# Optimization experiments

Measured on AMD Instinct MI355X. Metric: run time of the kernel, lower is better.

Reference implementation:

```python
import jax, jax.numpy as jnp
import numpy as np

FS, R, ULAW = 160, 2, 256  # frame_size, n_samples_per_step, 2**ulaw


def _conv1d(x, w, b):
    # x: [B,C,L], w: [O,I,3], VALID conv (PyTorch Conv1d, no padding)
    y = jax.lax.conv_general_dilated(x, w, (1,), 'VALID',
                                     dimension_numbers=('NCH', 'OIH', 'NCH'))
    return y + b[None, :, None]


def _gru(x, Wih, Whh, bih, bhh):
    # PyTorch GRU (batch_first), gate order r,z,n. x: [B,T,In] -> [B,T,H]
    B = x.shape[0]
    H = Whh.shape[1]
    xW = jnp.einsum('bti,gi->btg', x, Wih) + bih  # precompute input gates [B,T,3H]
    def step(h, xw):
        gh = h @ Whh.T + bhh
        r = jax.nn.sigmoid(xw[:, :H] + gh[:, :H])
        z = jax.nn.sigmoid(xw[:, H:2 * H] + gh[:, H:2 * H])
        n = jnp.tanh(xw[:, 2 * H:] + r * gh[:, 2 * H:])
        h = (1.0 - z) * n + z * h
        return h, h
    h0 = jnp.zeros((B, H), x.dtype)
    _, ys = jax.lax.scan(step, h0, jnp.swapaxes(xW, 0, 1))
    return jnp.swapaxes(ys, 0, 1)


def _mdense(x, w1, w2, b1, b2, f1, f2):
    return jnp.tanh(x @ w1.T + b1) * f1 + jnp.tanh(x @ w2.T + b2) * f2


def setup_inputs() -> dict:
    key = jax.random.key(0)
    ks = jax.random.split(key, 40)
    B, NF, NBF = 64, 15, 20
    T = (NF - 4) * FS  # 1760: two VALID k=3 convs -> 11 frames
    EP, ES, DF, H1, H2 = 64, 128, 128, 384, 16
    IN_A = 3 * ES * R + DF   # 896
    IN_B = H1 + DF           # 512
    p = lambda k, shape, s=0.1: (s * jax.random.normal(k, shape)).astype(jnp.float32)
    d = {
        'in_data': jax.random.randint(ks[0], (B, T, 3), 0, ULAW),
        'features': jax.random.normal(ks[1], (B, NF, NBF), jnp.float32),
        'periods': jax.random.randint(ks[2], (B, NF, 1), 0, 256),
        'targets': jax.random.randint(ks[3], (B, T), 0, ULAW),
        'embed_pitch': p(ks[4], (256, EP)),
        'embed_sig': p(ks[5], (ULAW, ES)),
        'conv1_w': p(ks[6], (DF, EP + NBF, 3)), 'conv1_b': p(ks[7], (DF,)),
        'conv2_w': p(ks[8], (DF, DF, 3)), 'conv2_b': p(ks[9], (DF,)),
        'fd1_w': p(ks[10], (DF, DF)), 'fd1_b': p(ks[11], (DF,)),
        'fd2_w': p(ks[12], (DF, DF)), 'fd2_b': p(ks[13], (DF,)),
        'ga_wih': p(ks[14], (3 * H1, IN_A)), 'ga_whh': p(ks[15], (3 * H1, H1)),
        'ga_bih': p(ks[16], (3 * H1,)), 'ga_bhh': p(ks[17], (3 * H1,)),
        'gb_wih': p(ks[18], (3 * H2, IN_B)), 'gb_whh': p(ks[19], (3 * H2, H2)),
        'gb_bih': p(ks[20], (3 * H2,)), 'gb_bhh': p(ks[21], (3 * H2,)),
        'md1_w1': p(ks[22], (ULAW, H2)), 'md1_w2': p(ks[23], (ULAW, H2)),
        'md1_b1': p(ks[24], (ULAW,)), 'md1_b2': p(ks[25], (ULAW,)),
        'md1_f1': jnp.ones((ULAW,), jnp.float32), 'md1_f2': jnp.ones((ULAW,), jnp.float32),
        'md2_w1': p(ks[26], (ULAW, H2 + ES)), 'md2_w2': p(ks[27], (ULAW, H2 + ES)),
        'md2_b1': p(ks[28], (ULAW,)), 'md2_b2': p(ks[29], (ULAW,)),
        'md2_f1': jnp.ones((ULAW,), jnp.float32), 'md2_f2': jnp.ones((ULAW,), jnp.float32),
    }
    return d


def reference(in_data, features, periods, targets, embed_pitch, embed_sig,
              conv1_w, conv1_b, conv2_w, conv2_b, fd1_w, fd1_b, fd2_w, fd2_b,
              ga_wih, ga_whh, ga_bih, ga_bhh, gb_wih, gb_whh, gb_bih, gb_bhh,
              md1_w1, md1_w2, md1_b1, md1_b2, md1_f1, md1_f2,
              md2_w1, md2_w2, md2_b1, md2_b2, md2_f1, md2_f2):
    B, T = targets.shape
    # frame-rate feature network
    pitch = embed_pitch[periods[..., 0]]                  # [B,15,EP]
    cat = jnp.concatenate([features, pitch], axis=-1)      # [B,15,NBF+EP]
    x = jnp.swapaxes(cat, 1, 2)                            # [B,C,15]
    x = jnp.tanh(_conv1d(x, conv1_w, conv1_b))
    x = jnp.tanh(_conv1d(x, conv2_w, conv2_b))             # [B,DF,11]
    f = jnp.swapaxes(x, 1, 2)
    f = jnp.tanh(f @ fd1_w.T + fd1_b)
    f = jnp.tanh(f @ fd2_w.T + fd2_b)                      # [B,11,DF]
    rep = jnp.repeat(f, FS // R, axis=1)                   # [B,880,DF]
    # sample-rate network (bunched: R samples per step)
    emb = embed_sig[in_data].reshape(B, T, -1).reshape(B, T // R, -1)  # [B,880,3*ES*R]
    rnn_in = jnp.concatenate([emb, rep], axis=-1)
    g1 = _gru(rnn_in, ga_wih, ga_whh, ga_bih, ga_bhh)      # [B,880,H1]
    g2 = _gru(jnp.concatenate([g1, rep], axis=-1), gb_wih, gb_whh, gb_bih, gb_bhh)  # [B,880,H2]
    o1 = _mdense(g2, md1_w1, md1_w2, md1_b1, md1_b2, md1_f1, md1_f2)  # [B,880,ULAW]
    # teacher forcing (p_teacher_forcing = 1.0): even-index targets feed branch 2
    pred_exc = targets[:, 0::R]                            # [B,880]
    ctx = jnp.concatenate([g2, embed_sig[pred_exc]], axis=-1)
    o2 = _mdense(ctx, md2_w1, md2_w2, md2_b1, md2_b2, md2_f1, md2_f2)
    # strided scatter: out[:, ::2]=o1, out[:, 1::2]=o2 == interleave
    out = jnp.stack([o1, o2], axis=2).reshape(B, T, ULAW)
    return out
```

## Files before the change

### kernel.cpp

```cpp
#include <hip/hip_runtime.h>
#include <hip/hip_bf16.h>
#include <hip/hip_fp16.h>

#define NF    15
#define NBF   20
#define TT    1760
#define TS    880
#define EP    64
#define ES    128
#define DF    128
#define H1    384
#define G3    1152
#define INA   896
#define JREP  11

typedef _Float16 h2v __attribute__((ext_vector_type(2)));

__device__ __forceinline__ float sigmf_(float x){ return 1.0f/(1.0f + __expf(-x)); }
__device__ __forceinline__ float tanhf_(float x){ return 2.0f/(1.0f + __expf(-2.0f*x)) - 1.0f; }
__device__ __forceinline__ h2v bc_h2(unsigned u){ return __builtin_bit_cast(h2v, u); }
__device__ __forceinline__ float fdot2_(h2v a, h2v b, float c){
#if __has_builtin(__builtin_amdgcn_fdot2)
  return __builtin_amdgcn_fdot2(a, b, c, false);
#else
  return c + (float)a[0]*(float)b[0] + (float)a[1]*(float)b[1];
#endif
}
__device__ __forceinline__ unsigned pk2_(float a, float b){
#if __has_builtin(__builtin_amdgcn_cvt_pkrtz)
  return __builtin_bit_cast(unsigned, __builtin_amdgcn_cvt_pkrtz(a, b));
#else
  unsigned lo = (unsigned)__builtin_bit_cast(unsigned short, (_Float16)a);
  unsigned hi = (unsigned)__builtin_bit_cast(unsigned short, (_Float16)b);
  return lo | (hi << 16);
#endif
}
__device__ __forceinline__ void bar_lgkm(){
  asm volatile("s_waitcnt lgkmcnt(0)" ::: "memory");
  __builtin_amdgcn_s_barrier();
  __builtin_amdgcn_sched_barrier(0);
}

__global__ __launch_bounds__(128) void k_frame(const float* feat, const int* periods, const float* embp,
   const float* c1w, const float* c1b, const float* c2w, const float* c2b,
   const float* f1w, const float* f1b, const float* f2w, const float* f2b, float* fout)
{
  __shared__ float cat[NF*84];
  __shared__ float x1[13*DF];
  __shared__ float x2[JREP*DF];
  int b = blockIdx.x, tid = threadIdx.x;
  for (int idx = tid; idx < NF*84; idx += 128){
    int j = idx/84, c = idx%84;
    cat[idx] = (c < NBF) ? feat[(b*NF+j)*NBF + c]
                         : embp[periods[b*NF+j]*EP + (c-NBF)];
  }
  __syncthreads();
  int o = tid;
  for (int p = 0; p < 13; ++p){
    float acc = c1b[o];
    for (int kk = 0; kk < 3; ++kk)
      for (int c = 0; c < 84; ++c)
        acc += cat[(p+kk)*84 + c] * c1w[(o*84+c)*3+kk];
    x1[p*DF+o] = tanhf_(acc);
  }
  __syncthreads();
  for (int p = 0; p < JREP; ++p){
    float acc = c2b[o];
    for (int kk = 0; kk < 3; ++kk)
      for (int c = 0; c < DF; ++c)
        acc += x1[(p+kk)*DF+c] * c2w[(o*DF+c)*3+kk];
    x2[p*DF+o] = tanhf_(acc);
  }
  __syncthreads();
  for (int p = 0; p < JREP; ++p){
    float acc = f1b[o];
    for (int c = 0; c < DF; ++c) acc += x2[p*DF+c]*f1w[o*DF+c];
    x1[p*DF+o] = tanhf_(acc);
  }
  __syncthreads();
  for (int p = 0; p < JREP; ++p){
    float acc = f2b[o];
    for (int c = 0; c < DF; ++c) acc += x1[p*DF+c]*f2w[o*DF+c];
    fout[(b*JREP+p)*DF+o] = tanhf_(acc);
  }
}

__global__ __launch_bounds__(256) void k_wpack5(const float* whh, _Float16* wpk){
  int o = blockIdx.x*256 + threadIdx.x;
  int hu = o & 1;
  int c  = (o >> 1) & 3;
  int idx = o >> 3;
  int tid = idx % 768;
  int n   = (idx / 768) % 18;
  int hf  = idx / (768*18);
  int i = tid % 384, u = tid / 384;
  int gd = n*4 + c;
  int m = gd / 12, dc = gd % 12;
  int pos  = (dc % 2) + 2*(dc / 6);
  int gate = (dc % 6) >> 1;
  int j = hf*96 + u*48 + (4*m + pos)*2 + hu;
  wpk[o] = (_Float16)whh[(gate*H1 + i)*H1 + j];
}

__global__ __launch_bounds__(256) void k_tables(const float* wih, const float* emb, float* GA){
  __shared__ float Wl[64*129];
  int k = blockIdx.x/18, g0 = (blockIdx.x%18)*64;
  int tid = threadIdx.x;
  for (int idx = tid; idx < 64*128; idx += 256){
    int gg = idx>>7, c = idx&127;
    Wl[gg*129+c] = wih[(size_t)(g0+gg)*INA + k*128 + c];
  }
  __syncthreads();
  int vv = tid>>6, gg = tid&63;
  for (int v = vv; v < 256; v += 4){
    const float* e = emb + (size_t)v*ES;
    float acc = 0.f;
    for (int c = 0; c < 128; ++c) acc += e[c]*Wl[gg*129+c];
    GA[(size_t)(k*256+v)*G3 + g0+gg] = acc;
  }
}

__global__ __launch_bounds__(256) void k_xwrepA(const float* wih, const float* f,
                                                const float* bih, const float* bhh, float* xwA){
  __shared__ float Wl[64*129];
  int g0 = blockIdx.x*64, tid = threadIdx.x;
  for (int idx = tid; idx < 64*128; idx += 256){
    int gg = idx>>7, c = idx&127;
    Wl[gg*129+c] = wih[(size_t)(g0+gg)*INA + 768 + c];
  }
  __syncthreads();
  int vv = tid>>6, gg = tid&63; int g = g0+gg;
  float badd = bih[g] + (g < 768 ? bhh[g] : 0.f);
  for (int row = vv; row < 64*JREP; row += 4){
    const float* fr = f + (size_t)row*DF;
    float acc = badd;
    for (int c = 0; c < 128; ++c) acc += fr[c]*Wl[gg*129+c];
    xwA[(size_t)row*G3 + g] = acc;
  }
}

__global__ __launch_bounds__(256) void k_xwrepB(const float* wih, const float* f,
                                                const float* bih, const float* bhh, float* xwB){
  __shared__ float Wl[48*129];
  int b = blockIdx.x, tid = threadIdx.x;
  for (int idx = tid; idx < 48*128; idx += 256){
    int r = idx>>7, c = idx&127;
    Wl[r*129+c] = wih[r*512 + 384 + c];
  }
  __syncthreads();
  for (int idx = tid; idx < JREP*48; idx += 256){
    int j = idx/48, r = idx%48;
    const float* fr = f + (size_t)(b*JREP+j)*DF;
    float acc = bih[r] + (r < 32 ? bhh[r] : 0.f);
    for (int c = 0; c < 128; ++c) acc += fr[c]*Wl[r*129+c];
    xwB[(size_t)(b*JREP+j)*48 + r] = acc;
  }
}

__global__ __launch_bounds__(256) void k_t2(const float* w1, const float* w2, const float* emb, float* T2){
  __shared__ float Wl[64*129];
  int tbl = blockIdx.x>>2; int c0 = (blockIdx.x&3)*64; int tid = threadIdx.x;
  const float* w = tbl ? w2 : w1;
  for (int idx = tid; idx < 64*128; idx += 256){
    int cc = idx>>7, e = idx&127;
    Wl[cc*129+e] = w[(c0+cc)*144 + 16 + e];
  }
  __syncthreads();
  int vv = tid>>6, cc = tid&63;
  for (int v = vv; v < 256; v += 4){
    const float* e = emb + (size_t)v*ES;
    float acc = 0.f;
    for (int c = 0; c < 128; ++c) acc += e[c]*Wl[cc*129+c];
    T2[tbl*65536 + v*256 + c0+cc] = acc;
  }
}

#define LD18(n) uint4 d##n = wsrc[(size_t)(n)*768];
#define Q2(A,B,C, q2) { \
  h2v hA = hh[jb2 + (q2)*2],     hB = hh[jb2 + (q2)*2 + 1]; \
  ar = fdot2_(hA, bc_h2(A.x), ar); ar = fdot2_(hB, bc_h2(A.y), ar); \
  az = fdot2_(hA, bc_h2(A.z), az); az = fdot2_(hB, bc_h2(A.w), az); \
  an = fdot2_(hA, bc_h2(B.x), an); an = fdot2_(hB, bc_h2(B.y), an); \
  h2v hC = hh[jb2 + (q2)*2 + 2], hD = hh[jb2 + (q2)*2 + 3]; \
  ar = fdot2_(hC, bc_h2(B.z), ar); ar = fdot2_(hD, bc_h2(B.w), ar); \
  az = fdot2_(hC, bc_h2(C.x), az); az = fdot2_(hD, bc_h2(C.y), az); \
  an = fdot2_(hC, bc_h2(C.z), an); an = fdot2_(hD, bc_h2(C.w), an); }
#define DOTS12 \
  Q2(d0,d1,d2,0) Q2(d3,d4,d5,2) Q2(d6,d7,d8,4) \
  Q2(d9,d10,d11,6) Q2(d12,d13,d14,8) Q2(d15,d16,d17,10)

#define PLW(n, p) { unsigned w = __hip_atomic_load((p), __ATOMIC_RELAXED, __HIP_MEMORY_SCOPE_AGENT); \
                    rv##n = w; ok &= ((w & 1023u) == tg); }

__global__ __launch_bounds__(768, 3) void k_scanA9(const int* __restrict__ in_data,
        const float* __restrict__ GA, const float* __restrict__ xwA,
        const uint4* __restrict__ wpk, const float* __restrict__ bhh,
        unsigned* __restrict__ g1u, unsigned* pbuf)
{
  __shared__ __align__(16) unsigned h16u[48];
  __shared__ __align__(8)  float pg[3][2][384];
  __shared__ __align__(8)  float xwb[2][G3];
  __shared__ int indr[2][8];
  const int P = blockIdx.x;
  const int b = P & 63, hf = P >> 6;
  const int tid = threadIdx.x;
  const int i  = tid % 384;
  const int u  = tid / 384;
  const int jb2 = u * 24;
  const int* ind_b = in_data + (size_t)b*TT*3;

  const uint4* wsrc = wpk + (size_t)(hf*18)*768 + tid;
  LD18(0) LD18(1) LD18(2) LD18(3) LD18(4) LD18(5) LD18(6) LD18(7) LD18(8)
  LD18(9) LD18(10) LD18(11) LD18(12) LD18(13) LD18(14) LD18(15) LD18(16) LD18(17)

  const bool isGat = (tid < 576);
  const int  c0 = 2*tid, c1 = 2*tid + 1;
  const bool isPub = (tid >= 96 && tid < 672);
  const int  po0 = 2*(tid - 96);

  float hreg0 = 0.f, hreg1 = 0.f, bn0 = 0.f, bn1 = 0.f;
  if (tid < 48){
    bn0 = bhh[768 + hf*96 + 2*tid];
    bn1 = bhh[768 + hf*96 + 2*tid + 1];
    h16u[tid] = 0u;
  }
  if (isGat){
    float s0 = xwA[(size_t)(b*JREP)*G3 + c0];
    float s1 = xwA[(size_t)(b*JREP)*G3 + c1];
    #pragma unroll
    for (int k2 = 0; k2 < 6; ++k2){
      int v = ind_b[k2];
      s0 += GA[((size_t)k2*256 + v)*G3 + c0];
      s1 += GA[((size_t)k2*256 + v)*G3 + c1];
    }
    xwb[0][c0] = s0; xwb[0][c1] = s1;
  }
  if (tid >= 576 && tid < 582) indr[1][tid-576] = ind_b[6 + (tid-576)];

  unsigned* pbo = pbuf + ((size_t)(b*4 + hf)*2)*G3;
  const int pf1 = (hf+1)&3, pf2 = (hf+2)&3, pf3 = (hf+3)&3;
  const unsigned* pb1 = pbuf + ((size_t)(b*4 + pf1)*2)*G3 + hf*96 + 2*(tid<48?tid:0);
  const unsigned* pb2 = pbuf + ((size_t)(b*4 + pf2)*2)*G3 + hf*96 + 2*(tid<48?tid:0);
  const unsigned* pb3 = pbuf + ((size_t)(b*4 + pf3)*2)*G3 + hf*96 + 2*(tid<48?tid:0);
  const h2v* hh = (const h2v*)h16u;
  __syncthreads();

  for (int t = 0; t < TS; ++t){
    const int nb = t & 1;
    const int tp = t + 1;
    float ga0=0.f,ga1=0.f,ga2=0.f,ga3=0.f,ga4=0.f,ga5=0.f,gx0=0.f;
    float gb0=0.f,gb1=0.f,gb2=0.f,gb3=0.f,gb4=0.f,gb5=0.f,gx1=0.f;
    if (tp < TS && isGat){
      int v0=indr[tp&1][0], v1=indr[tp&1][1], v2=indr[tp&1][2];
      int v3=indr[tp&1][3], v4=indr[tp&1][4], v5=indr[tp&1][5];
      const float* xwr = xwA + ((size_t)(b*JREP) + tp/80)*G3;
      ga0 = GA[((size_t)0*256 + v0)*G3 + c0]; gb0 = GA[((size_t)0*256 + v0)*G3 + c1];
      ga1 = GA[((size_t)1*256 + v1)*G3 + c0]; gb1 = GA[((size_t)1*256 + v1)*G3 + c1];
      ga2 = GA[((size_t)2*256 + v2)*G3 + c0]; gb2 = GA[((size_t)2*256 + v2)*G3 + c1];
      ga3 = GA[((size_t)3*256 + v3)*G3 + c0]; gb3 = GA[((size_t)3*256 + v3)*G3 + c1];
      ga4 = GA[((size_t)4*256 + v4)*G3 + c0]; gb4 = GA[((size_t)4*256 + v4)*G3 + c1];
      ga5 = GA[((size_t)5*256 + v5)*G3 + c0]; gb5 = GA[((size_t)5*256 + v5)*G3 + c1];
      gx0 = xwr[c0]; gx1 = xwr[c1];
    }
    int iv = 0;
    const int stg = t + 2;
    const bool doStg = (tid >= 576 && tid < 582 && stg < TS);
    if (doStg) iv = ind_b[6*stg + (tid-576)];
    float ar=0.f, az=0.f, an=0.f;
    DOTS12
    pg[0][u][i] = ar; pg[1][u][i] = az; pg[2][u][i] = an;
    if (tp < TS && isGat){
      xwb[tp&1][c0] = ga0+ga1+ga2+ga3+ga4+ga5+gx0;
      xwb[tp&1][c1] = gb0+gb1+gb2+gb3+gb4+gb5+gx1;
    }
    if (doStg) indr[t&1][tid-576] = iv;
    bar_lgkm();
    if (isPub){
      int g = po0/384, ii = po0 - g*384;
      float2 p0 = *(const float2*)&pg[g][0][ii];
      float2 p1 = *(const float2*)&pg[g][1][ii];
      float v0 = p0.x + p1.x, v1 = p0.y + p1.y;
      unsigned tw0 = (__builtin_bit_cast(unsigned, v0) & 0xFFFFFC00u) | (unsigned)t;
      unsigned tw1 = (__builtin_bit_cast(unsigned, v1) & 0xFFFFFC00u) | (unsigned)t;
      unsigned* dst = pbo + (size_t)nb*G3 + po0;
      __hip_atomic_store(dst,     tw0, __ATOMIC_RELAXED, __HIP_MEMORY_SCOPE_AGENT);
      __hip_atomic_store(dst + 1, tw1, __ATOMIC_RELAXED, __HIP_MEMORY_SCOPE_AGENT);
    } else if (tid < 48){
      const unsigned tg = (unsigned)t;
      const unsigned* q1 = pb1 + (size_t)nb*G3;
      const unsigned* q2 = pb2 + (size_t)nb*G3;
      const unsigned* q3 = pb3 + (size_t)nb*G3;
      unsigned rv0,rv1,rv2,rv3,rv4,rv5,rv6,rv7,rv8;
      unsigned rv9,rv10,rv11,rv12,rv13,rv14,rv15,rv16,rv17;
      bool ok;
      do {
        ok = true;
        PLW(0,  q1+0) PLW(1,  q1+1) PLW(2,  q1+384) PLW(3,  q1+385) PLW(4,  q1+768) PLW(5,  q1+769)
        PLW(6,  q2+0) PLW(7,  q2+1) PLW(8,  q2+384) PLW(9,  q2+385) PLW(10, q2+768) PLW(11, q2+769)
        PLW(12, q3+0) PLW(13, q3+1) PLW(14, q3+384) PLW(15, q3+385) PLW(16, q3+768) PLW(17, q3+769)
        if (!ok) __builtin_amdgcn_s_sleep(1);
      } while (!ok);
      __builtin_amdgcn_sched_barrier(0);
      #define FV(n) __builtin_bit_cast(float, rv##n & 0xFFFFFC00u)
      int i0 = hf*96 + 2*tid;
      float2 o0 = *(const float2*)&pg[0][0][i0];  float2 o0b = *(const float2*)&pg[0][1][i0];
      float2 o1 = *(const float2*)&pg[1][0][i0];  float2 o1b = *(const float2*)&pg[1][1][i0];
      float2 o2 = *(const float2*)&pg[2][0][i0];  float2 o2b = *(const float2*)&pg[2][1][i0];
      float2 xr = *(const float2*)&xwb[nb][i0];
      float2 xz = *(const float2*)&xwb[nb][384 + i0];
      float2 xn = *(const float2*)&xwb[nb][768 + i0];
      float R0 = o0.x + o0b.x + FV(0)  + FV(6)  + FV(12) + xr.x;
      float R1 = o0.y + o0b.y + FV(1)  + FV(7)  + FV(13) + xr.y;
      float Z0 = o1.x + o1b.x + FV(2)  + FV(8)  + FV(14) + xz.x;
      float Z1 = o1.y + o1b.y + FV(3)  + FV(9)  + FV(15) + xz.y;
      float G0 = o2.x + o2b.x + FV(4)  + FV(10) + FV(16) + bn0;
      float G1 = o2.y + o2b.y + FV(5)  + FV(11) + FV(17) + bn1;
      #undef FV
      float rr0 = sigmf_(R0), zz0 = sigmf_(Z0);
      float nn0 = tanhf_(xn.x + rr0*G0);
      float h0 = (1.f - zz0)*nn0 + zz0*hreg0; hreg0 = h0;
      float rr1 = sigmf_(R1), zz1 = sigmf_(Z1);
      float nn1 = tanhf_(xn.y + rr1*G1);
      float h1 = (1.f - zz1)*nn1 + zz1*hreg1; hreg1 = h1;
      unsigned pack = pk2_(h0, h1);
      h16u[tid] = pack;
      g1u[((size_t)b*TS + t)*192 + hf*48 + tid] = pack;
    }
    bar_lgkm();
  }
}

__global__ __launch_bounds__(256) void k_xwB(const _Float16* g1, const float* wih,
                                             const float* xwrB, float* xwB){
  __shared__ _Float16 gl[16*392];
  int bi = blockIdx.x; int b = bi/55; int t0 = (bi%55)*16; int tid = threadIdx.x;
  for (int idx = tid; idx < 16*H1; idx += 256){
    int tt = idx/H1, c = idx%H1;
    gl[tt*392+c] = g1[((size_t)b*TS + t0+tt)*H1 + c];
  }
  __syncthreads();
  int rr = tid>>4, tt = tid&15;
  int t = t0+tt;
  const float* xr = xwrB + ((size_t)(b*JREP) + t/80)*48;
  for (int rb = 0; rb < 3; ++rb){
    int r = rb*16 + rr;
    const float* wrow = wih + (size_t)r*512;
    float acc = 0.f;
    for (int c = 0; c < H1; ++c) acc += (float)gl[tt*392+c]*wrow[c];
    xwB[((size_t)b*TS + t)*48 + r] = acc + xr[r];
  }
}

__global__ __launch_bounds__(64) void k_scanB(const float* xwB, const float* whh,
                                              const float* bhh, float* g2){
  __shared__ float wl[48*17];
  __shared__ float h2s[16];
  __shared__ float pre[32];
  __shared__ float xn[16], gn[16];
  int b = blockIdx.x, tid = threadIdx.x;
  for (int idx = tid; idx < 768; idx += 64) wl[(idx>>4)*17 + (idx&15)] = whh[idx];
  if (tid < 16) h2s[tid] = 0.f;
  float bn = (tid >= 32 && tid < 48) ? bhh[tid] : 0.f;
  __syncthreads();
  for (int t = 0; t < TS; ++t){
    if (tid < 48){
      float xw = xwB[((size_t)b*TS + t)*48 + tid];
      float gh = 0.f;
      for (int e = 0; e < 16; ++e) gh += wl[tid*17+e]*h2s[e];
      if (tid < 32) pre[tid] = xw + gh;
      else { xn[tid-32] = xw; gn[tid-32] = gh + bn; }
    }
    __syncthreads();
    if (tid < 16){
      float r = sigmf_(pre[tid]), z = sigmf_(pre[16+tid]);
      float n = tanhf_(xn[tid] + r*gn[tid]);
      float hn = (1.f - z)*n + z*h2s[tid];
      h2s[tid] = hn;
      g2[((size_t)b*TS + t)*16 + tid] = hn;
    }
    __syncthreads();
  }
}

__global__ __launch_bounds__(256) void k_out(const float* g2, const int* targets, const float* T2,
    const float* m1w1, const float* m1w2, const float* m1b1, const float* m1b2,
    const float* m1f1, const float* m1f2,
    const float* m2w1, const float* m2w2, const float* m2b1, const float* m2b2,
    const float* m2f1, const float* m2f2, float* out)
{
  __shared__ float wA[256*17], wB[256*17], wC[256*17], wD[256*17];
  __shared__ float g2l[16*16];
  int bi = blockIdx.x; int b = bi/55; int t0 = (bi%55)*16; int c = threadIdx.x;
  for (int d = 0; d < 16; ++d){
    wA[c*17+d] = m1w1[c*16+d];  wB[c*17+d] = m1w2[c*16+d];
    wC[c*17+d] = m2w1[c*144+d]; wD[c*17+d] = m2w2[c*144+d];
  }
  { int tt = c>>4, d = c&15; g2l[c] = g2[((size_t)b*TS + t0+tt)*16 + d]; }
  __syncthreads();
  float b1a = m1b1[c], b2a = m1b2[c], f1a = m1f1[c], f2a = m1f2[c];
  float b1b = m2b1[c], b2b = m2b2[c], f1b = m2f1[c], f2b = m2f2[c];
  for (int tt = 0; tt < 16; ++tt){
    int t = t0+tt;
    float d1 = b1a, d2 = b2a, e1 = b1b, e2 = b2b;
    for (int d = 0; d < 16; ++d){
      float g = g2l[tt*16+d];
      d1 += g*wA[c*17+d]; d2 += g*wB[c*17+d];
      e1 += g*wC[c*17+d]; e2 += g*wD[c*17+d];
    }
    int v = targets[b*TT + 2*t];
    e1 += T2[v*256+c]; e2 += T2[65536 + v*256+c];
    float o1 = f1a*tanhf_(d1) + f2a*tanhf_(d2);
    float o2 = f1b*tanhf_(e1) + f2b*tanhf_(e2);
    size_t base = ((size_t)b*TS + t)*2*256;
    out[base + c]       = o1;
    out[base + 256 + c] = o2;
  }
}

extern "C" void kernel_launch(void* const* d_in, const int* in_sizes, int n_in,
                              void* d_out, int out_size, void* d_ws, size_t ws_size,
                              hipStream_t stream) {
  const int*   in_data = (const int*)  d_in[0];
  const float* feat    = (const float*)d_in[1];
  const int*   periods = (const int*)  d_in[2];
  const int*   targets = (const int*)  d_in[3];
  const float* embp    = (const float*)d_in[4];
  const float* embs    = (const float*)d_in[5];
  const float* c1w = (const float*)d_in[6];  const float* c1b = (const float*)d_in[7];
  const float* c2w = (const float*)d_in[8];  const float* c2b = (const float*)d_in[9];
  const float* f1w = (const float*)d_in[10]; const float* f1b = (const float*)d_in[11];
  const float* f2w = (const float*)d_in[12]; const float* f2b = (const float*)d_in[13];
  const float* ga_wih = (const float*)d_in[14]; const float* ga_whh = (const float*)d_in[15];
  const float* ga_bih = (const float*)d_in[16]; const float* ga_bhh = (const float*)d_in[17];
  const float* gb_wih = (const float*)d_in[18]; const float* gb_whh = (const float*)d_in[19];
  const float* gb_bih = (const float*)d_in[20]; const float* gb_bhh = (const float*)d_in[21];
  const float* m1w1 = (const float*)d_in[22]; const float* m1w2 = (const float*)d_in[23];
  const float* m1b1 = (const float*)d_in[24]; const float* m1b2 = (const float*)d_in[25];
  const float* m1f1 = (const float*)d_in[26]; const float* m1f2 = (const float*)d_in[27];
  const float* m2w1 = (const float*)d_in[28]; const float* m2w2 = (const float*)d_in[29];
  const float* m2b1 = (const float*)d_in[30]; const float* m2b2 = (const float*)d_in[31];
  const float* m2f1 = (const float*)d_in[32]; const float* m2f2 = (const float*)d_in[33];
  float* out = (float*)d_out;

  float* GA     = (float*)d_ws;
  float* xWrepA = GA     + 1769472;
  float* xWrepB = xWrepA + 811008;
  float* fbuf   = xWrepB + 33792;
  float* xWB    = fbuf   + 90112;
  float* g2buf  = xWB    + 2703360;
  float* T2     = g2buf  + 901120;
  _Float16* Wpk = (_Float16*)(T2 + 131072);
  unsigned* pbuf = (unsigned*)(Wpk + 442368);
  _Float16* g1  = (_Float16*)d_out;

  (void)hipMemsetAsync(pbuf, 0xFF, 589824*sizeof(unsigned), stream);
  hipLaunchKernelGGL(k_frame, dim3(64), dim3(128), 0, stream,
                     feat, periods, embp, c1w, c1b, c2w, c2b, f1w, f1b, f2w, f2b, fbuf);
  hipLaunchKernelGGL(k_wpack5, dim3(1728), dim3(256), 0, stream, ga_whh, Wpk);
  hipLaunchKernelGGL(k_tables, dim3(108), dim3(256), 0, stream, ga_wih, embs, GA);
  hipLaunchKernelGGL(k_t2, dim3(8), dim3(256), 0, stream, m2w1, m2w2, embs, T2);
  hipLaunchKernelGGL(k_xwrepA, dim3(18), dim3(256), 0, stream, ga_wih, fbuf, ga_bih, ga_bhh, xWrepA);
  hipLaunchKernelGGL(k_xwrepB, dim3(64), dim3(256), 0, stream, gb_wih, fbuf, gb_bih, gb_bhh, xWrepB);
  hipLaunchKernelGGL(k_scanA9, dim3(256), dim3(768), 0, stream,
                     in_data, GA, xWrepA, (const uint4*)Wpk, ga_bhh,
                     (unsigned*)g1, pbuf);
  hipLaunchKernelGGL(k_xwB, dim3(64*55), dim3(256), 0, stream, g1, gb_wih, xWrepB, xWB);
  hipLaunchKernelGGL(k_scanB, dim3(64), dim3(64), 0, stream, xWB, gb_whh, gb_bhh, g2buf);
  hipLaunchKernelGGL(k_out, dim3(64*55), dim3(256), 0, stream,
                     g2buf, targets, T2, m1w1, m1w2, m1b1, m1b2, m1f1, m1f2,
                     m2w1, m2w2, m2b1, m2b2, m2f1, m2f2, out);
}
```

Baseline: 4.094 ms.

## Pack cross-block partial sums contiguously and poll with vector loads; fdot2 in xwB

The GRU-A scan now has each publisher write only the partial-gate values a given peer block needs, laid out contiguously per destination lane. Each consumer lane can then poll its three peers with one dwordx4 plus one dwordx2 load each (inline asm, sc1) instead of 18 scalar atomic loads. This cuts polling latency on the serial per-step critical path. Separately, k_xwB stages fp16-packed weights in LDS and uses fdot2 on packed g1, and k_scanB prefetches the next step's input gates. The inline-asm cache-coherence flags and the new layout add correctness risk across blocks.

```diff
diff --git a/kernel.cpp b/kernel.cpp
--- a/kernel.cpp
+++ b/kernel.cpp
@@ -177,6 +177,16 @@
 
 #define LD18(n) uint4 d##n = wsrc[(size_t)(n)*768];
 #define Q2(A,B,C, q2) { \
+  h2v hA = hh[jb2 + (q2)*2],     h2v_hB; h2v_hB = hh[jb2 + (q2)*2 + 1]; h2v hB = h2v_hB; \
+  ar = fdot2_(hA, bc_h2(A.x), ar); ar = fdot2_(hB, bc_h2(A.y), ar); \
+  az = fdot2_(hA, bc_h2(A.z), az); az = fdot2_(hB, bc_h2(A.w), az); \
+  an = fdot2_(hA, bc_h2(B.x), an); an = fdot2_(hB, bc_h2(B.y), an); \
+  h2v hC = hh[jb2 + (q2)*2 + 2], hD = hh[jb2 + (q2)*2 + 3]; \
+  ar = fdot2_(hC, bc_h2(B.z), ar); ar = fdot2_(hD, bc_h2(B.w), ar); \
+  az = fdot2_(hC, bc_h2(C.x), az); az = fdot2_(hD, bc_h2(C.y), az); \
+  an = fdot2_(hC, bc_h2(C.z), an); an = fdot2_(hD, bc_h2(C.w), an); }
+#undef Q2
+#define Q2(A,B,C, q2) { \
   h2v hA = hh[jb2 + (q2)*2],     hB = hh[jb2 + (q2)*2 + 1]; \
   ar = fdot2_(hA, bc_h2(A.x), ar); ar = fdot2_(hB, bc_h2(A.y), ar); \
   az = fdot2_(hA, bc_h2(A.z), az); az = fdot2_(hB, bc_h2(A.w), az); \
@@ -189,10 +199,7 @@
   Q2(d0,d1,d2,0) Q2(d3,d4,d5,2) Q2(d6,d7,d8,4) \
   Q2(d9,d10,d11,6) Q2(d12,d13,d14,8) Q2(d15,d16,d17,10)
 
-#define PLW(n, p) { unsigned w = __hip_atomic_load((p), __ATOMIC_RELAXED, __HIP_MEMORY_SCOPE_AGENT); \
-                    rv##n = w; ok &= ((w & 1023u) == tg); }
-
-__global__ __launch_bounds__(768, 3) void k_scanA9(const int* __restrict__ in_data,
+__global__ __launch_bounds__(768, 3) void k_scanA10(const int* __restrict__ in_data,
         const float* __restrict__ GA, const float* __restrict__ xwA,
         const uint4* __restrict__ wpk, const float* __restrict__ bhh,
         unsigned* __restrict__ g1u, unsigned* pbuf)
@@ -215,8 +222,15 @@
 
   const bool isGat = (tid < 576);
   const int  c0 = 2*tid, c1 = 2*tid + 1;
-  const bool isPub = (tid >= 96 && tid < 672);
-  const int  po0 = 2*(tid - 96);
+  const bool isPub = (tid >= 96 && tid < 528);
+  int pubRel=0, pubL=0, pubWp=0, pubR0=0;
+  if (isPub){
+    int e = tid - 96;
+    pubRel = e / 144; int p = e % 144;
+    pubL = p / 3; pubWp = p % 3;
+    int qp = (hf + 1 + pubRel) & 3;
+    pubR0 = qp*96 + 2*pubL;
+  }
 
   float hreg0 = 0.f, hreg1 = 0.f, bn0 = 0.f, bn1 = 0.f;
   if (tid < 48){
@@ -238,10 +252,9 @@
   if (tid >= 576 && tid < 582) indr[1][tid-576] = ind_b[6 + (tid-576)];
 
   unsigned* pbo = pbuf + ((size_t)(b*4 + hf)*2)*G3;
-  const int pf1 = (hf+1)&3, pf2 = (hf+2)&3, pf3 = (hf+3)&3;
-  const unsigned* pb1 = pbuf + ((size_t)(b*4 + pf1)*2)*G3 + hf*96 + 2*(tid<48?tid:0);
-  const unsigned* pb2 = pbuf + ((size_t)(b*4 + pf2)*2)*G3 + hf*96 + 2*(tid<48?tid:0);
-  const unsigned* pb3 = pbuf + ((size_t)(b*4 + pf3)*2)*G3 + hf*96 + 2*(tid<48?tid:0);
+  const unsigned* s1b = pbuf + ((size_t)(b*4 + ((hf+1)&3))*2)*G3 + 2*384 + (tid<48?tid:0)*8;
+  const unsigned* s2b = pbuf + ((size_t)(b*4 + ((hf+2)&3))*2)*G3 + 1*384 + (tid<48?tid:0)*8;
+  const unsigned* s3b = pbuf + ((size_t)(b*4 + ((hf+3)&3))*2)*G3 + 0*384 + (tid<48?tid:0)*8;
   const h2v* hh = (const h2v*)h16u;
   __syncthreads();
 
@@ -276,32 +289,15 @@
     if (doStg) indr[t&1][tid-576] = iv;
     bar_lgkm();
     if (isPub){
-      int g = po0/384, ii = po0 - g*384;
-      float2 p0 = *(const float2*)&pg[g][0][ii];
-      float2 p1 = *(const float2*)&pg[g][1][ii];
-      float v0 = p0.x + p1.x, v1 = p0.y + p1.y;
-      unsigned tw0 = (__builtin_bit_cast(unsigned, v0) & 0xFFFFFC00u) | (unsigned)t;
-      unsigned tw1 = (__builtin_bit_cast(unsigned, v1) & 0xFFFFFC00u) | (unsigned)t;
-      unsigned* dst = pbo + (size_t)nb*G3 + po0;
+      float v0 = pg[pubWp][0][pubR0]   + pg[pubWp][1][pubR0];
+      float v1 = pg[pubWp][0][pubR0+1] + pg[pubWp][1][pubR0+1];
+      unsigned tw0 = (__builtin_bit_cast(unsigned, v0) & 0xFFFFFC00u) | (unsigned)(t & 1023);
+      unsigned tw1 = (__builtin_bit_cast(unsigned, v1) & 0xFFFFFC00u) | (unsigned)(t & 1023);
+      unsigned* dst = pbo + (size_t)nb*G3 + pubRel*384 + pubL*8 + pubWp*2;
       __hip_atomic_store(dst,     tw0, __ATOMIC_RELAXED, __HIP_MEMORY_SCOPE_AGENT);
       __hip_atomic_store(dst + 1, tw1, __ATOMIC_RELAXED, __HIP_MEMORY_SCOPE_AGENT);
-    } else if (tid < 48){
-      const unsigned tg = (unsigned)t;
-      const unsigned* q1 = pb1 + (size_t)nb*G3;
-      const unsigned* q2 = pb2 + (size_t)nb*G3;
-      const unsigned* q3 = pb3 + (size_t)nb*G3;
-      unsigned rv0,rv1,rv2,rv3,rv4,rv5,rv6,rv7,rv8;
-      unsigned rv9,rv10,rv11,rv12,rv13,rv14,rv15,rv16,rv17;
-      bool ok;
-      do {
-        ok = true;
-        PLW(0,  q1+0) PLW(1,  q1+1) PLW(2,  q1+384) PLW(3,  q1+385) PLW(4,  q1+768) PLW(5,  q1+769)
-        PLW(6,  q2+0) PLW(7,  q2+1) PLW(8,  q2+384) PLW(9,  q2+385) PLW(10, q2+768) PLW(11, q2+769)
-        PLW(12, q3+0) PLW(13, q3+1) PLW(14, q3+384) PLW(15, q3+385) PLW(16, q3+768) PLW(17, q3+769)
-        if (!ok) __builtin_amdgcn_s_sleep(1);
-      } while (!ok);
-      __builtin_amdgcn_sched_barrier(0);
-      #define FV(n) __builtin_bit_cast(float, rv##n & 0xFFFFFC00u)
+    }
+    if (tid < 48){
       int i0 = hf*96 + 2*tid;
       float2 o0 = *(const float2*)&pg[0][0][i0];  float2 o0b = *(const float2*)&pg[0][1][i0];
       float2 o1 = *(const float2*)&pg[1][0][i0];  float2 o1b = *(const float2*)&pg[1][1][i0];
@@ -309,12 +305,40 @@
       float2 xr = *(const float2*)&xwb[nb][i0];
       float2 xz = *(const float2*)&xwb[nb][384 + i0];
       float2 xn = *(const float2*)&xwb[nb][768 + i0];
-      float R0 = o0.x + o0b.x + FV(0)  + FV(6)  + FV(12) + xr.x;
-      float R1 = o0.y + o0b.y + FV(1)  + FV(7)  + FV(13) + xr.y;
-      float Z0 = o1.x + o1b.x + FV(2)  + FV(8)  + FV(14) + xz.x;
-      float Z1 = o1.y + o1b.y + FV(3)  + FV(9)  + FV(15) + xz.y;
-      float G0 = o2.x + o2b.x + FV(4)  + FV(10) + FV(16) + bn0;
-      float G1 = o2.y + o2b.y + FV(5)  + FV(11) + FV(17) + bn1;
+      const unsigned tg = (unsigned)t & 1023u;
+      const unsigned* q1 = s1b + (size_t)nb*G3;
+      const unsigned* q2 = s2b + (size_t)nb*G3;
+      const unsigned* q3 = s3b + (size_t)nb*G3;
+      uint4 A1,A2,A3; uint2 B1,B2,B3;
+      bool ok;
+      do {
+        asm volatile(
+          "global_load_dwordx4 %0, %6, off sc1\n\t"
+          "global_load_dwordx2 %1, %6, off offset:16 sc1\n\t"
+          "global_load_dwordx4 %2, %7, off sc1\n\t"
+          "global_load_dwordx2 %3, %7, off offset:16 sc1\n\t"
+          "global_load_dwordx4 %4, %8, off sc1\n\t"
+          "global_load_dwordx2 %5, %8, off offset:16 sc1\n\t"
+          "s_waitcnt vmcnt(0)"
+          : "=&v"(A1),"=&v"(B1),"=&v"(A2),"=&v"(B2),"=&v"(A3),"=&v"(B3)
+          : "v"(q1),"v"(q2),"v"(q3) : "memory");
+        __builtin_amdgcn_sched_barrier(0);
+        ok = ((A1.x&1023u)==tg) & ((A1.y&1023u)==tg) & ((A1.z&1023u)==tg) & ((A1.w&1023u)==tg)
+           & ((B1.x&1023u)==tg) & ((B1.y&1023u)==tg)
+           & ((A2.x&1023u)==tg) & ((A2.y&1023u)==tg) & ((A2.z&1023u)==tg) & ((A2.w&1023u)==tg)
+           & ((B2.x&1023u)==tg) & ((B2.y&1023u)==tg)
+           & ((A3.x&1023u)==tg) & ((A3.y&1023u)==tg) & ((A3.z&1023u)==tg) & ((A3.w&1023u)==tg)
+           & ((B3.x&1023u)==tg) & ((B3.y&1023u)==tg);
+        if (!ok) __builtin_amdgcn_s_sleep(2);
+      } while (!ok);
+      __builtin_amdgcn_sched_barrier(0);
+      #define FV(w) __builtin_bit_cast(float, (w) & 0xFFFFFC00u)
+      float R0 = o0.x + o0b.x + FV(A1.x) + FV(A2.x) + FV(A3.x) + xr.x;
+      float R1 = o0.y + o0b.y + FV(A1.y) + FV(A2.y) + FV(A3.y) + xr.y;
+      float Z0 = o1.x + o1b.x + FV(A1.z) + FV(A2.z) + FV(A3.z) + xz.x;
+      float Z1 = o1.y + o1b.y + FV(A1.w) + FV(A2.w) + FV(A3.w) + xz.y;
+      float G0 = o2.x + o2b.x + FV(B1.x) + FV(B2.x) + FV(B3.x) + bn0;
+      float G1 = o2.y + o2b.y + FV(B1.y) + FV(B2.y) + FV(B3.y) + bn1;
       #undef FV
       float rr0 = sigmf_(R0), zz0 = sigmf_(Z0);
       float nn0 = tanhf_(xn.x + rr0*G0);
@@ -330,23 +354,30 @@
   }
 }
 
-__global__ __launch_bounds__(256) void k_xwB(const _Float16* g1, const float* wih,
+__global__ __launch_bounds__(256) void k_xwB(const unsigned* g1u, const float* wih,
                                              const float* xwrB, float* xwB){
-  __shared__ _Float16 gl[16*392];
+  __shared__ __align__(16) unsigned gl[16*194];
+  __shared__ __align__(16) unsigned wl[48*194];
   int bi = blockIdx.x; int b = bi/55; int t0 = (bi%55)*16; int tid = threadIdx.x;
-  for (int idx = tid; idx < 16*H1; idx += 256){
-    int tt = idx/H1, c = idx%H1;
-    gl[tt*392+c] = g1[((size_t)b*TS + t0+tt)*H1 + c];
+  for (int idx = tid; idx < 48*192; idx += 256){
+    int r = idx/192, cp = idx%192;
+    wl[r*194+cp] = pk2_(wih[r*512 + 2*cp], wih[r*512 + 2*cp + 1]);
+  }
+  for (int idx = tid; idx < 16*192; idx += 256){
+    int tt = idx/192, c = idx%192;
+    gl[tt*194+c] = g1u[((size_t)b*TS + t0+tt)*192 + c];
   }
   __syncthreads();
   int rr = tid>>4, tt = tid&15;
   int t = t0+tt;
   const float* xr = xwrB + ((size_t)(b*JREP) + t/80)*48;
+  const h2v* gp = (const h2v*)&gl[tt*194];
   for (int rb = 0; rb < 3; ++rb){
     int r = rb*16 + rr;
-    const float* wrow = wih + (size_t)r*512;
+    const h2v* wp_ = (const h2v*)&wl[r*194];
     float acc = 0.f;
-    for (int c = 0; c < H1; ++c) acc += (float)gl[tt*392+c]*wrow[c];
+    #pragma unroll 8
+    for (int c = 0; c < 192; ++c) acc = fdot2_(gp[c], wp_[c], acc);
     xwB[((size_t)b*TS + t)*48 + r] = acc + xr[r];
   }
 }
@@ -361,11 +392,14 @@
   for (int idx = tid; idx < 768; idx += 64) wl[(idx>>4)*17 + (idx&15)] = whh[idx];
   if (tid < 16) h2s[tid] = 0.f;
   float bn = (tid >= 32 && tid < 48) ? bhh[tid] : 0.f;
+  float xw_n = (tid < 48) ? xwB[(size_t)b*TS*48 + tid] : 0.f;
   __syncthreads();
   for (int t = 0; t < TS; ++t){
+    float xw = xw_n;
+    if (t+1 < TS && tid < 48) xw_n = xwB[((size_t)b*TS + t+1)*48 + tid];
     if (tid < 48){
-      float xw = xwB[((size_t)b*TS + t)*48 + tid];
       float gh = 0.f;
+      #pragma unroll
       for (int e = 0; e < 16; ++e) gh += wl[tid*17+e]*h2s[e];
       if (tid < 32) pre[tid] = xw + gh;
       else { xn[tid-32] = xw; gn[tid-32] = gh + bn; }
@@ -461,10 +495,11 @@
   hipLaunchKernelGGL(k_t2, dim3(8), dim3(256), 0, stream, m2w1, m2w2, embs, T2);
   hipLaunchKernelGGL(k_xwrepA, dim3(18), dim3(256), 0, stream, ga_wih, fbuf, ga_bih, ga_bhh, xWrepA);
   hipLaunchKernelGGL(k_xwrepB, dim3(64), dim3(256), 0, stream, gb_wih, fbuf, gb_bih, gb_bhh, xWrepB);
-  hipLaunchKernelGGL(k_scanA9, dim3(256), dim3(768), 0, stream,
+  hipLaunchKernelGGL(k_scanA10, dim3(256), dim3(768), 0, stream,
                      in_data, GA, xWrepA, (const uint4*)Wpk, ga_bhh,
                      (unsigned*)g1, pbuf);
-  hipLaunchKernelGGL(k_xwB, dim3(64*55), dim3(256), 0, stream, g1, gb_wih, xWrepB, xWB);
+  hipLaunchKernelGGL(k_xwB, dim3(64*55), dim3(256), 0, stream,
+                     (const unsigned*)g1, gb_wih, xWrepB, xWB);
   hipLaunchKernelGGL(k_scanB, dim3(64), dim3(64), 0, stream, xWB, gb_whh, gb_bhh, g2buf);
   hipLaunchKernelGGL(k_out, dim3(64*55), dim3(256), 0, stream,
                      g2buf, targets, T2, m1w1, m1w2, m1b1, m1b2, m1f1, m1f2,
```

Result: slower. 4.869 ms (+18.9%).

## Add fast cross-block exchange path with probe, fp16 dot xwB, prefetch scanB inputs

Applied to the files above, without the earlier changes.

The GRU-A scan now publishes partial gate sums twice: once with agent-scope atomics and once with sc0 vector stores into a second buffer. At startup each block probes whether its neighbour block is visibly co-resident through the sc0 path. If so, it polls that buffer with batched dwordx2 loads and falls back to the atomic path after a bounded number of attempts. The aim is to cut the latency of the per-step inter-block handshake. Separately, k_xwB now packs its weights into fp16 pairs in shared memory and uses fdot2, and k_scanB prefetches the next step's input. The extra stores, memsets and probe add overhead, and relying on sc0 coherence for visibility is risky.

```diff
diff --git a/kernel.cpp b/kernel.cpp
--- a/kernel.cpp
+++ b/kernel.cpp
@@ -192,15 +192,16 @@
 #define PLW(n, p) { unsigned w = __hip_atomic_load((p), __ATOMIC_RELAXED, __HIP_MEMORY_SCOPE_AGENT); \
                     rv##n = w; ok &= ((w & 1023u) == tg); }
 
-__global__ __launch_bounds__(768, 3) void k_scanA9(const int* __restrict__ in_data,
+__global__ __launch_bounds__(768, 3) void k_scanA11(const int* __restrict__ in_data,
         const float* __restrict__ GA, const float* __restrict__ xwA,
         const uint4* __restrict__ wpk, const float* __restrict__ bhh,
-        unsigned* __restrict__ g1u, unsigned* pbuf)
+        unsigned* __restrict__ g1u, unsigned* pbuf, unsigned* pbufF, int* probeF)
 {
   __shared__ __align__(16) unsigned h16u[48];
   __shared__ __align__(8)  float pg[3][2][384];
   __shared__ __align__(8)  float xwb[2][G3];
   __shared__ int indr[2][8];
+  __shared__ int fastFlag;
   const int P = blockIdx.x;
   const int b = P & 63, hf = P >> 6;
   const int tid = threadIdx.x;
@@ -212,6 +213,21 @@
   const uint4* wsrc = wpk + (size_t)(hf*18)*768 + tid;
   LD18(0) LD18(1) LD18(2) LD18(3) LD18(4) LD18(5) LD18(6) LD18(7) LD18(8)
   LD18(9) LD18(10) LD18(11) LD18(12) LD18(13) LD18(14) LD18(15) LD18(16) LD18(17)
+
+  if (tid == 0){
+    unsigned s = 0x5A5A5A5Au;
+    asm volatile("global_store_dword %0, %1, off sc0" :: "v"(probeF + P), "v"(s) : "memory");
+    int pk = ((hf+1)&3)*64 + b;
+    int seen = 0;
+    for (int it = 0; it < 2000 && !seen; ++it){
+      int v;
+      asm volatile("global_load_dword %0, %1, off sc0\n\ts_waitcnt vmcnt(0)"
+                   : "=v"(v) : "v"(probeF + pk) : "memory");
+      if (v == (int)0x5A5A5A5Au) seen = 1;
+      else __builtin_amdgcn_s_sleep(2);
+    }
+    fastFlag = seen;
+  }
 
   const bool isGat = (tid < 576);
   const int  c0 = 2*tid, c1 = 2*tid + 1;
@@ -237,13 +253,18 @@
   }
   if (tid >= 576 && tid < 582) indr[1][tid-576] = ind_b[6 + (tid-576)];
 
-  unsigned* pbo = pbuf + ((size_t)(b*4 + hf)*2)*G3;
-  const int pf1 = (hf+1)&3, pf2 = (hf+2)&3, pf3 = (hf+3)&3;
-  const unsigned* pb1 = pbuf + ((size_t)(b*4 + pf1)*2)*G3 + hf*96 + 2*(tid<48?tid:0);
-  const unsigned* pb2 = pbuf + ((size_t)(b*4 + pf2)*2)*G3 + hf*96 + 2*(tid<48?tid:0);
-  const unsigned* pb3 = pbuf + ((size_t)(b*4 + pf3)*2)*G3 + hf*96 + 2*(tid<48?tid:0);
+  unsigned* pbo  = pbuf  + ((size_t)(b*4 + hf)*2)*G3;
+  unsigned* pboF = pbufF + ((size_t)(b*4 + hf)*2)*G3;
+  const int lidx = (tid < 48 ? tid : 0);
+  const unsigned* pb1  = pbuf  + ((size_t)(b*4 + ((hf+1)&3))*2)*G3 + hf*96 + 2*lidx;
+  const unsigned* pb2  = pbuf  + ((size_t)(b*4 + ((hf+2)&3))*2)*G3 + hf*96 + 2*lidx;
+  const unsigned* pb3  = pbuf  + ((size_t)(b*4 + ((hf+3)&3))*2)*G3 + hf*96 + 2*lidx;
+  const unsigned* pb1F = pbufF + ((size_t)(b*4 + ((hf+1)&3))*2)*G3 + hf*96 + 2*lidx;
+  const unsigned* pb2F = pbufF + ((size_t)(b*4 + ((hf+2)&3))*2)*G3 + hf*96 + 2*lidx;
+  const unsigned* pb3F = pbufF + ((size_t)(b*4 + ((hf+3)&3))*2)*G3 + hf*96 + 2*lidx;
   const h2v* hh = (const h2v*)h16u;
   __syncthreads();
+  bool myFast = (fastFlag != 0);
 
   for (int t = 0; t < TS; ++t){
     const int nb = t & 1;
@@ -280,28 +301,16 @@
       float2 p0 = *(const float2*)&pg[g][0][ii];
       float2 p1 = *(const float2*)&pg[g][1][ii];
       float v0 = p0.x + p1.x, v1 = p0.y + p1.y;
-      unsigned tw0 = (__builtin_bit_cast(unsigned, v0) & 0xFFFFFC00u) | (unsigned)t;
-      unsigned tw1 = (__builtin_bit_cast(unsigned, v1) & 0xFFFFFC00u) | (unsigned)t;
+      unsigned tw0 = (__builtin_bit_cast(unsigned, v0) & 0xFFFFFC00u) | (unsigned)(t & 1023);
+      unsigned tw1 = (__builtin_bit_cast(unsigned, v1) & 0xFFFFFC00u) | (unsigned)(t & 1023);
+      uint2 twv; twv.x = tw0; twv.y = tw1;
+      unsigned* dstF = pboF + (size_t)nb*G3 + po0;
+      asm volatile("global_store_dwordx2 %0, %1, off sc0" :: "v"(dstF), "v"(twv) : "memory");
       unsigned* dst = pbo + (size_t)nb*G3 + po0;
       __hip_atomic_store(dst,     tw0, __ATOMIC_RELAXED, __HIP_MEMORY_SCOPE_AGENT);
       __hip_atomic_store(dst + 1, tw1, __ATOMIC_RELAXED, __HIP_MEMORY_SCOPE_AGENT);
-    } else if (tid < 48){
-      const unsigned tg = (unsigned)t;
-      const unsigned* q1 = pb1 + (size_t)nb*G3;
-      const unsigned* q2 = pb2 + (size_t)nb*G3;
-      const unsigned* q3 = pb3 + (size_t)nb*G3;
-      unsigned rv0,rv1,rv2,rv3,rv4,rv5,rv6,rv7,rv8;
-      unsigned rv9,rv10,rv11,rv12,rv13,rv14,rv15,rv16,rv17;
-      bool ok;
-      do {
-        ok = true;
-        PLW(0,  q1+0) PLW(1,  q1+1) PLW(2,  q1+384) PLW(3,  q1+385) PLW(4,  q1+768) PLW(5,  q1+769)
-        PLW(6,  q2+0) PLW(7,  q2+1) PLW(8,  q2+384) PLW(9,  q2+385) PLW(10, q2+768) PLW(11, q2+769)
-        PLW(12, q3+0) PLW(13, q3+1) PLW(14, q3+384) PLW(15, q3+385) PLW(16, q3+768) PLW(17, q3+769)
-        if (!ok) __builtin_amdgcn_s_sleep(1);
-      } while (!ok);
-      __builtin_amdgcn_sched_barrier(0);
-      #define FV(n) __builtin_bit_cast(float, rv##n & 0xFFFFFC00u)
+    }
+    if (tid < 48){
       int i0 = hf*96 + 2*tid;
       float2 o0 = *(const float2*)&pg[0][0][i0];  float2 o0b = *(const float2*)&pg[0][1][i0];
       float2 o1 = *(const float2*)&pg[1][0][i0];  float2 o1b = *(const float2*)&pg[1][1][i0];
@@ -309,13 +318,68 @@
       float2 xr = *(const float2*)&xwb[nb][i0];
       float2 xz = *(const float2*)&xwb[nb][384 + i0];
       float2 xn = *(const float2*)&xwb[nb][768 + i0];
-      float R0 = o0.x + o0b.x + FV(0)  + FV(6)  + FV(12) + xr.x;
-      float R1 = o0.y + o0b.y + FV(1)  + FV(7)  + FV(13) + xr.y;
-      float Z0 = o1.x + o1b.x + FV(2)  + FV(8)  + FV(14) + xz.x;
-      float Z1 = o1.y + o1b.y + FV(3)  + FV(9)  + FV(15) + xz.y;
-      float G0 = o2.x + o2b.x + FV(4)  + FV(10) + FV(16) + bn0;
-      float G1 = o2.y + o2b.y + FV(5)  + FV(11) + FV(17) + bn1;
-      #undef FV
+      const unsigned tg = (unsigned)t & 1023u;
+      unsigned rv0,rv1,rv2,rv3,rv4,rv5,rv6,rv7,rv8;
+      unsigned rv9,rv10,rv11,rv12,rv13,rv14,rv15,rv16,rv17;
+      bool got = false;
+      if (myFast){
+        const unsigned* q1 = pb1F + (size_t)nb*G3;
+        const unsigned* q2 = pb2F + (size_t)nb*G3;
+        const unsigned* q3 = pb3F + (size_t)nb*G3;
+        for (int att = 0; att < 32 && !got; ++att){
+          uint2 F10,F11,F12,F20,F21,F22,F30,F31,F32;
+          asm volatile(
+            "global_load_dwordx2 %0, %9, off sc0\n\t"
+            "global_load_dwordx2 %1, %9, off offset:1536 sc0\n\t"
+            "global_load_dwordx2 %2, %9, off offset:3072 sc0\n\t"
+            "global_load_dwordx2 %3, %10, off sc0\n\t"
+            "global_load_dwordx2 %4, %10, off offset:1536 sc0\n\t"
+            "global_load_dwordx2 %5, %10, off offset:3072 sc0\n\t"
+            "global_load_dwordx2 %6, %11, off sc0\n\t"
+            "global_load_dwordx2 %7, %11, off offset:1536 sc0\n\t"
+            "global_load_dwordx2 %8, %11, off offset:3072 sc0\n\t"
+            "s_waitcnt vmcnt(0)"
+            : "=&v"(F10),"=&v"(F11),"=&v"(F12),"=&v"(F20),"=&v"(F21),"=&v"(F22),
+              "=&v"(F30),"=&v"(F31),"=&v"(F32)
+            : "v"(q1),"v"(q2),"v"(q3) : "memory");
+          __builtin_amdgcn_sched_barrier(0);
+          bool ok = ((F10.x&1023u)==tg)&((F10.y&1023u)==tg)&((F11.x&1023u)==tg)&((F11.y&1023u)==tg)
+                  & ((F12.x&1023u)==tg)&((F12.y&1023u)==tg)
+                  & ((F20.x&1023u)==tg)&((F20.y&1023u)==tg)&((F21.x&1023u)==tg)&((F21.y&1023u)==tg)
+                  & ((F22.x&1023u)==tg)&((F22.y&1023u)==tg)
+                  & ((F30.x&1023u)==tg)&((F30.y&1023u)==tg)&((F31.x&1023u)==tg)&((F31.y&1023u)==tg)
+                  & ((F32.x&1023u)==tg)&((F32.y&1023u)==tg);
+          if (ok){
+            rv0=F10.x; rv1=F10.y; rv2=F11.x; rv3=F11.y; rv4=F12.x; rv5=F12.y;
+            rv6=F20.x; rv7=F20.y; rv8=F21.x; rv9=F21.y; rv10=F22.x; rv11=F22.y;
+            rv12=F30.x; rv13=F30.y; rv14=F31.x; rv15=F31.y; rv16=F32.x; rv17=F32.y;
+            got = true;
+          } else __builtin_amdgcn_s_sleep(2);
+        }
+        if (!got) myFast = false;
+      }
+      if (!got){
+        const unsigned* q1 = pb1 + (size_t)nb*G3;
+        const unsigned* q2 = pb2 + (size_t)nb*G3;
+        const unsigned* q3 = pb3 + (size_t)nb*G3;
+        bool ok;
+        do {
+          ok = true;
+          PLW(0,  q1+0) PLW(1,  q1+1) PLW(2,  q1+384) PLW(3,  q1+385) PLW(4,  q1+768) PLW(5,  q1+769)
+          PLW(6,  q2+0) PLW(7,  q2+1) PLW(8,  q2+384) PLW(9,  q2+385) PLW(10, q2+768) PLW(11, q2+769)
+          PLW(12, q3+0) PLW(13, q3+1) PLW(14, q3+384) PLW(15, q3+385) PLW(16, q3+768) PLW(17, q3+769)
+          if (!ok) __builtin_amdgcn_s_sleep(1);
+        } while (!ok);
+      }
+      __builtin_amdgcn_sched_barrier(0);
+      #define FVV(n) __builtin_bit_cast(float, rv##n & 0xFFFFFC00u)
+      float R0 = o0.x + o0b.x + FVV(0)  + FVV(6)  + FVV(12) + xr.x;
+      float R1 = o0.y + o0b.y + FVV(1)  + FVV(7)  + FVV(13) + xr.y;
+      float Z0 = o1.x + o1b.x + FVV(2)  + FVV(8)  + FVV(14) + xz.x;
+      float Z1 = o1.y + o1b.y + FVV(3)  + FVV(9)  + FVV(15) + xz.y;
+      float G0 = o2.x + o2b.x + FVV(4)  + FVV(10) + FVV(16) + bn0;
+      float G1 = o2.y + o2b.y + FVV(5)  + FVV(11) + FVV(17) + bn1;
+      #undef FVV
       float rr0 = sigmf_(R0), zz0 = sigmf_(Z0);
       float nn0 = tanhf_(xn.x + rr0*G0);
       float h0 = (1.f - zz0)*nn0 + zz0*hreg0; hreg0 = h0;
@@ -330,23 +394,30 @@
   }
 }
 
-__global__ __launch_bounds__(256) void k_xwB(const _Float16* g1, const float* wih,
+__global__ __launch_bounds__(256) void k_xwB(const unsigned* g1u, const float* wih,
                                              const float* xwrB, float* xwB){
-  __shared__ _Float16 gl[16*392];
+  __shared__ __align__(16) unsigned gl[16*194];
+  __shared__ __align__(16) unsigned wl[48*194];
   int bi = blockIdx.x; int b = bi/55; int t0 = (bi%55)*16; int tid = threadIdx.x;
-  for (int idx = tid; idx < 16*H1; idx += 256){
-    int tt = idx/H1, c = idx%H1;
-    gl[tt*392+c] = g1[((size_t)b*TS + t0+tt)*H1 + c];
+  for (int idx = tid; idx < 48*192; idx += 256){
+    int r = idx/192, cp = idx%192;
+    wl[r*194+cp] = pk2_(wih[r*512 + 2*cp], wih[r*512 + 2*cp + 1]);
+  }
+  for (int idx = tid; idx < 16*192; idx += 256){
+    int tt = idx/192, c = idx%192;
+    gl[tt*194+c] = g1u[((size_t)b*TS + t0+tt)*192 + c];
   }
   __syncthreads();
   int rr = tid>>4, tt = tid&15;
   int t = t0+tt;
   const float* xr = xwrB + ((size_t)(b*JREP) + t/80)*48;
+  const h2v* gp = (const h2v*)&gl[tt*194];
   for (int rb = 0; rb < 3; ++rb){
     int r = rb*16 + rr;
-    const float* wrow = wih + (size_t)r*512;
+    const h2v* wp_ = (const h2v*)&wl[r*194];
     float acc = 0.f;
-    for (int c = 0; c < H1; ++c) acc += (float)gl[tt*392+c]*wrow[c];
+    #pragma unroll 8
+    for (int c = 0; c < 192; ++c) acc = fdot2_(gp[c], wp_[c], acc);
     xwB[((size_t)b*TS + t)*48 + r] = acc + xr[r];
   }
 }
@@ -361,11 +432,14 @@
   for (int idx = tid; idx < 768; idx += 64) wl[(idx>>4)*17 + (idx&15)] = whh[idx];
   if (tid < 16) h2s[tid] = 0.f;
   float bn = (tid >= 32 && tid < 48) ? bhh[tid] : 0.f;
+  float xw_n = (tid < 48) ? xwB[(size_t)b*TS*48 + tid] : 0.f;
   __syncthreads();
   for (int t = 0; t < TS; ++t){
+    float xw = xw_n;
+    if (t+1 < TS && tid < 48) xw_n = xwB[((size_t)b*TS + t+1)*48 + tid];
     if (tid < 48){
-      float xw = xwB[((size_t)b*TS + t)*48 + tid];
       float gh = 0.f;
+      #pragma unroll
       for (int e = 0; e < 16; ++e) gh += wl[tid*17+e]*h2s[e];
       if (tid < 32) pre[tid] = xw + gh;
       else { xn[tid-32] = xw; gn[tid-32] = gh + bn; }
@@ -450,10 +524,14 @@
   float* g2buf  = xWB    + 2703360;
   float* T2     = g2buf  + 901120;
   _Float16* Wpk = (_Float16*)(T2 + 131072);
-  unsigned* pbuf = (unsigned*)(Wpk + 442368);
+  unsigned* pbuf  = (unsigned*)(Wpk + 442368);
+  unsigned* pbufF = pbuf + 589824;
+  int* probeF     = (int*)(pbufF + 589824);
   _Float16* g1  = (_Float16*)d_out;
 
   (void)hipMemsetAsync(pbuf, 0xFF, 589824*sizeof(unsigned), stream);
+  (void)hipMemsetAsync(pbufF, 0xFF, 589824*sizeof(unsigned), stream);
+  (void)hipMemsetAsync(probeF, 0, 256*sizeof(int), stream);
   hipLaunchKernelGGL(k_frame, dim3(64), dim3(128), 0, stream,
                      feat, periods, embp, c1w, c1b, c2w, c2b, f1w, f1b, f2w, f2b, fbuf);
   hipLaunchKernelGGL(k_wpack5, dim3(1728), dim3(256), 0, stream, ga_whh, Wpk);
@@ -461,10 +539,11 @@
   hipLaunchKernelGGL(k_t2, dim3(8), dim3(256), 0, stream, m2w1, m2w2, embs, T2);
   hipLaunchKernelGGL(k_xwrepA, dim3(18), dim3(256), 0, stream, ga_wih, fbuf, ga_bih, ga_bhh, xWrepA);
   hipLaunchKernelGGL(k_xwrepB, dim3(64), dim3(256), 0, stream, gb_wih, fbuf, gb_bih, gb_bhh, xWrepB);
-  hipLaunchKernelGGL(k_scanA9, dim3(256), dim3(768), 0, stream,
+  hipLaunchKernelGGL(k_scanA11, dim3(256), dim3(768), 0, stream,
                      in_data, GA, xWrepA, (const uint4*)Wpk, ga_bhh,
-                     (unsigned*)g1, pbuf);
-  hipLaunchKernelGGL(k_xwB, dim3(64*55), dim3(256), 0, stream, g1, gb_wih, xWrepB, xWB);
+                     (unsigned*)g1, pbuf, pbufF, probeF);
+  hipLaunchKernelGGL(k_xwB, dim3(64*55), dim3(256), 0, stream,
+                     (const unsigned*)g1, gb_wih, xWrepB, xWB);
   hipLaunchKernelGGL(k_scanB, dim3(64), dim3(64), 0, stream, xWB, gb_whh, gb_bhh, g2buf);
   hipLaunchKernelGGL(k_out, dim3(64*55), dim3(256), 0, stream,
                      g2buf, targets, T2, m1w1, m1w2, m1b1, m1b2, m1f1, m1f2,
```

New measurement: 4.165 ms. About the same (+1.7%).
